# Kernel tuning notes

Hardware: AMD Instinct MI355X
Metric: run time of the kernel (lower is better)

## Reference

```python
import jax, jax.numpy as jnp
import numpy as np

N_NODES = 100000
N_EDGES = 3200000
INPUT_DIM = 16
HIDDEN_DIM = 8


def setup_inputs() -> dict:
    key = jax.random.key(0)
    k1, k2, k3, k4 = jax.random.split(key, 4)
    x = jax.random.normal(k1, (N_NODES, INPUT_DIM), dtype=jnp.float32)
    edge_index = jax.random.randint(k2, (2, N_EDGES), 0, N_NODES, dtype=jnp.int64)
    # PyTorch Linear default init: U(-1/sqrt(fan_in), 1/sqrt(fan_in)); scaled normal is fine for a reference
    W1 = jax.random.normal(k3, (2 * INPUT_DIM, HIDDEN_DIM), dtype=jnp.float32) / np.sqrt(2 * INPUT_DIM)
    b1 = jnp.zeros((HIDDEN_DIM,), dtype=jnp.float32)
    W2 = jax.random.normal(k4, (HIDDEN_DIM, 1), dtype=jnp.float32) / np.sqrt(HIDDEN_DIM)
    b2 = jnp.zeros((1,), dtype=jnp.float32)
    return {"x": x, "edge_index": edge_index, "W1": W1, "b1": b1, "W2": W2, "b2": b2}


def reference(x, edge_index, W1, b1, W2, b2):
    row, col = edge_index[0], edge_index[1]
    # B = cat([x[col], x[row]], dim=-1).detach()  -> [E, 2*input_dim]
    B = jax.lax.stop_gradient(jnp.concatenate([x[col], x[row]], axis=-1))
    h = jnp.tanh(B @ W1 + b1)            # [E, hidden_dim]
    out = jax.nn.sigmoid(h @ W2 + b2)    # [E, 1]
    return out
```

## Files before the change

### kernel.cpp

```cpp
#include <hip/hip_runtime.h>

#define IN_DIM 16
#define HID 8

__device__ __forceinline__ float fast_tanh(float z) {
    float e = __expf(2.0f * z);
    return 1.0f - 2.0f * __builtin_amdgcn_rcpf(e + 1.0f);
}

__global__ __launch_bounds__(256) void node_pre(
    const float* __restrict__ x, const float* __restrict__ W1,
    const float* __restrict__ b1, float* __restrict__ u,
    float* __restrict__ v, int n_nodes)
{
    __shared__ float sW[2 * IN_DIM * HID];
    __shared__ float sb[HID];
    int t = threadIdx.x;
    if (t < 2 * IN_DIM * HID) sW[t] = W1[t];
    if (t < HID) sb[t] = b1[t];
    __syncthreads();
    int n = blockIdx.x * 256 + t;
    if (n >= n_nodes) return;

    const float4* xp = (const float4*)(x + (size_t)n * IN_DIM);
    float xr[IN_DIM];
    float4 a;
    a = xp[0]; xr[0]=a.x;  xr[1]=a.y;  xr[2]=a.z;  xr[3]=a.w;
    a = xp[1]; xr[4]=a.x;  xr[5]=a.y;  xr[6]=a.z;  xr[7]=a.w;
    a = xp[2]; xr[8]=a.x;  xr[9]=a.y;  xr[10]=a.z; xr[11]=a.w;
    a = xp[3]; xr[12]=a.x; xr[13]=a.y; xr[14]=a.z; xr[15]=a.w;

    float au[HID], av[HID];
    #pragma unroll
    for (int j = 0; j < HID; j++) { au[j] = sb[j]; av[j] = 0.0f; }
    #pragma unroll
    for (int k = 0; k < IN_DIM; k++) {
        #pragma unroll
        for (int j = 0; j < HID; j++) {
            au[j] = fmaf(xr[k], sW[k * HID + j], au[j]);
            av[j] = fmaf(xr[k], sW[(IN_DIM + k) * HID + j], av[j]);
        }
    }
    float4* up = (float4*)(u + (size_t)n * HID);
    float4* vp = (float4*)(v + (size_t)n * HID);
    up[0] = make_float4(au[0], au[1], au[2], au[3]);
    up[1] = make_float4(au[4], au[5], au[6], au[7]);
    vp[0] = make_float4(av[0], av[1], av[2], av[3]);
    vp[1] = make_float4(av[4], av[5], av[6], av[7]);
}

__global__ __launch_bounds__(256) void edge_k(
    const int* __restrict__ idx, const float* __restrict__ u,
    const float* __restrict__ v, const float* __restrict__ W2,
    const float* __restrict__ b2, float* __restrict__ out, int n_edges)
{
    __shared__ float sw2[HID];
    __shared__ float sb2;
    int t = threadIdx.x;
    if (t < HID) sw2[t] = W2[t];
    if (t == 0) sb2 = b2[0];
    __syncthreads();

    int e = blockIdx.x * 256 + t;
    if (e >= n_edges) return;

    int row = idx[e];
    int col = idx[n_edges + e];

    const float4* up = (const float4*)(u + (size_t)col * HID);
    const float4* vp = (const float4*)(v + (size_t)row * HID);
    float4 u0 = up[0], u1 = up[1];
    float4 v0 = vp[0], v1 = vp[1];

    float s = sb2;
    s = fmaf(fast_tanh(u0.x + v0.x), sw2[0], s);
    s = fmaf(fast_tanh(u0.y + v0.y), sw2[1], s);
    s = fmaf(fast_tanh(u0.z + v0.z), sw2[2], s);
    s = fmaf(fast_tanh(u0.w + v0.w), sw2[3], s);
    s = fmaf(fast_tanh(u1.x + v1.x), sw2[4], s);
    s = fmaf(fast_tanh(u1.y + v1.y), sw2[5], s);
    s = fmaf(fast_tanh(u1.z + v1.z), sw2[6], s);
    s = fmaf(fast_tanh(u1.w + v1.w), sw2[7], s);

    float es = __expf(-s);
    out[e] = __builtin_amdgcn_rcpf(1.0f + es);
}

extern "C" void kernel_launch(void* const* d_in, const int* in_sizes, int n_in,
                              void* d_out, int out_size, void* d_ws, size_t ws_size,
                              hipStream_t stream) {
    const float* x  = (const float*)d_in[0];
    const int*   idx = (const int*)d_in[1];
    const float* W1 = (const float*)d_in[2];
    const float* b1 = (const float*)d_in[3];
    const float* W2 = (const float*)d_in[4];
    const float* b2 = (const float*)d_in[5];
    float* out = (float*)d_out;

    int n_nodes = in_sizes[0] / IN_DIM;
    int n_edges = in_sizes[1] / 2;

    float* u = (float*)d_ws;
    float* v = u + (size_t)n_nodes * HID;

    node_pre<<<(n_nodes + 255) / 256, 256, 0, stream>>>(x, W1, b1, u, v, n_nodes);
    edge_k<<<(n_edges + 255) / 256, 256, 0, stream>>>(idx, u, v, W2, b2, out, n_edges);
}
```

Before: 145.1 us.

## Store node projections as fp16 interleaved and process four edges per thread

Node-side projections u and v are now stored as half precision and interleaved per node in one 32-byte record, which halves gather traffic and puts both halves in one line. The edge kernel now handles four edges per thread using vectorized nontemporal index loads and output stores, so more gathers are in flight per thread. The cost is fp16 rounding of pre-activations, which may loosen accuracy, plus a scalar tail path for leftover edges.

```diff
diff --git a/kernel.cpp b/kernel.cpp
--- a/kernel.cpp
+++ b/kernel.cpp
@@ -1,7 +1,11 @@
 #include <hip/hip_runtime.h>
+#include <hip/hip_fp16.h>
 
 #define IN_DIM 16
 #define HID 8
+
+typedef int   v4i __attribute__((ext_vector_type(4)));
+typedef float v4f __attribute__((ext_vector_type(4)));
 
 __device__ __forceinline__ float fast_tanh(float z) {
     float e = __expf(2.0f * z);
@@ -10,8 +14,7 @@
 
 __global__ __launch_bounds__(256) void node_pre(
     const float* __restrict__ x, const float* __restrict__ W1,
-    const float* __restrict__ b1, float* __restrict__ u,
-    float* __restrict__ v, int n_nodes)
+    const float* __restrict__ b1, __half* __restrict__ uv, int n_nodes)
 {
     __shared__ float sW[2 * IN_DIM * HID];
     __shared__ float sb[HID];
@@ -41,18 +44,37 @@
             av[j] = fmaf(xr[k], sW[(IN_DIM + k) * HID + j], av[j]);
         }
     }
-    float4* up = (float4*)(u + (size_t)n * HID);
-    float4* vp = (float4*)(v + (size_t)n * HID);
-    up[0] = make_float4(au[0], au[1], au[2], au[3]);
-    up[1] = make_float4(au[4], au[5], au[6], au[7]);
-    vp[0] = make_float4(av[0], av[1], av[2], av[3]);
-    vp[1] = make_float4(av[4], av[5], av[6], av[7]);
+    union { __half2 h[4]; float4 f; } pu, pv;
+    #pragma unroll
+    for (int i = 0; i < 4; i++) {
+        pu.h[i] = __floats2half2_rn(au[2*i], au[2*i+1]);
+        pv.h[i] = __floats2half2_rn(av[2*i], av[2*i+1]);
+    }
+    float4* o = (float4*)(uv + (size_t)n * 16);
+    o[0] = pu.f;
+    o[1] = pv.f;
+}
+
+__device__ __forceinline__ float edge_eval(float4 uf, float4 vf,
+                                           const float* sw2, float sb2)
+{
+    union { float4 f; __half2 h[4]; } U, V;
+    U.f = uf; V.f = vf;
+    float s = sb2;
+    #pragma unroll
+    for (int i = 0; i < 4; i++) {
+        float2 a = __half22float2(U.h[i]);
+        float2 b = __half22float2(V.h[i]);
+        s = fmaf(fast_tanh(a.x + b.x), sw2[2*i],   s);
+        s = fmaf(fast_tanh(a.y + b.y), sw2[2*i+1], s);
+    }
+    return __builtin_amdgcn_rcpf(1.0f + __expf(-s));
 }
 
 __global__ __launch_bounds__(256) void edge_k(
-    const int* __restrict__ idx, const float* __restrict__ u,
-    const float* __restrict__ v, const float* __restrict__ W2,
-    const float* __restrict__ b2, float* __restrict__ out, int n_edges)
+    const int* __restrict__ idx, const __half* __restrict__ uv,
+    const float* __restrict__ W2, const float* __restrict__ b2,
+    float* __restrict__ out, int n_edges)
 {
     __shared__ float sw2[HID];
     __shared__ float sb2;
@@ -60,30 +82,33 @@
     if (t < HID) sw2[t] = W2[t];
     if (t == 0) sb2 = b2[0];
     __syncthreads();
+    float lb2 = sb2;
 
-    int e = blockIdx.x * 256 + t;
-    if (e >= n_edges) return;
+    long e0 = ((long)blockIdx.x * 256 + t) * 4;
+    if (e0 + 4 <= n_edges) {
+        v4i rows = __builtin_nontemporal_load((const v4i*)(idx + e0));
+        v4i cols = __builtin_nontemporal_load((const v4i*)(idx + n_edges + e0));
 
-    int row = idx[e];
-    int col = idx[n_edges + e];
+        const float4* uvp = (const float4*)uv;
+        float4 u0 = uvp[2*(size_t)cols.x],     u1 = uvp[2*(size_t)cols.y];
+        float4 u2 = uvp[2*(size_t)cols.z],     u3 = uvp[2*(size_t)cols.w];
+        float4 w0 = uvp[2*(size_t)rows.x + 1], w1 = uvp[2*(size_t)rows.y + 1];
+        float4 w2 = uvp[2*(size_t)rows.z + 1], w3 = uvp[2*(size_t)rows.w + 1];
 
-    const float4* up = (const float4*)(u + (size_t)col * HID);
-    const float4* vp = (const float4*)(v + (size_t)row * HID);
-    float4 u0 = up[0], u1 = up[1];
-    float4 v0 = vp[0], v1 = vp[1];
-
-    float s = sb2;
-    s = fmaf(fast_tanh(u0.x + v0.x), sw2[0], s);
-    s = fmaf(fast_tanh(u0.y + v0.y), sw2[1], s);
-    s = fmaf(fast_tanh(u0.z + v0.z), sw2[2], s);
-    s = fmaf(fast_tanh(u0.w + v0.w), sw2[3], s);
-    s = fmaf(fast_tanh(u1.x + v1.x), sw2[4], s);
-    s = fmaf(fast_tanh(u1.y + v1.y), sw2[5], s);
-    s = fmaf(fast_tanh(u1.z + v1.z), sw2[6], s);
-    s = fmaf(fast_tanh(u1.w + v1.w), sw2[7], s);
-
-    float es = __expf(-s);
-    out[e] = __builtin_amdgcn_rcpf(1.0f + es);
+        v4f r;
+        r.x = edge_eval(u0, w0, sw2, lb2);
+        r.y = edge_eval(u1, w1, sw2, lb2);
+        r.z = edge_eval(u2, w2, sw2, lb2);
+        r.w = edge_eval(u3, w3, sw2, lb2);
+        __builtin_nontemporal_store(r, (v4f*)(out + e0));
+    } else {
+        const float4* uvp = (const float4*)uv;
+        for (long e = e0; e < n_edges; e++) {
+            int row = idx[e];
+            int col = idx[n_edges + e];
+            out[e] = edge_eval(uvp[2*(size_t)col], uvp[2*(size_t)row + 1], sw2, lb2);
+        }
+    }
 }
 
 extern "C" void kernel_launch(void* const* d_in, const int* in_sizes, int n_in,
@@ -100,9 +125,9 @@
     int n_nodes = in_sizes[0] / IN_DIM;
     int n_edges = in_sizes[1] / 2;
 
-    float* u = (float*)d_ws;
-    float* v = u + (size_t)n_nodes * HID;
+    __half* uv = (__half*)d_ws;
 
-    node_pre<<<(n_nodes + 255) / 256, 256, 0, stream>>>(x, W1, b1, u, v, n_nodes);
-    edge_k<<<(n_edges + 255) / 256, 256, 0, stream>>>(idx, u, v, W2, b2, out, n_edges);
+    node_pre<<<(n_nodes + 255) / 256, 256, 0, stream>>>(x, W1, b1, uv, n_nodes);
+    int epb = 256 * 4;
+    edge_k<<<(n_edges + epb - 1) / epb, 256, 0, stream>>>(idx, uv, W2, b2, out, n_edges);
 }
```

New measurement: 118.5 us. 18.4% less time.
